# Optimization experiments

Hardware: AMD Instinct MI355X
Metric: run time of the kernel (lower is better)

Reference implementation:

```python
import jax, jax.numpy as jnp
import numpy as np

ALPHA = 0.9
EPS = 1e-5
SEQ, BATCH, D_MODEL, FF_DIM = 2048, 16, 512, 2048


def _layer_norm(x, g, b):
    m = jnp.mean(x, axis=-1, keepdims=True)
    v = jnp.mean((x - m) ** 2, axis=-1, keepdims=True)
    return (x - m) * jax.lax.rsqrt(v + EPS) * g + b


def _decay_matrix(seq, dtype):
    # Closed form of the torch roll/flip/tril loop:
    #   W[i, j] = alpha^{i-j+1}            for j <= i
    #   W[i, i] += 1 - sum_{k=1}^{i+1} alpha^k   (diag correction)
    i = jnp.arange(seq)
    diff = i[:, None] - i[None, :]                       # [S, S]
    causal = diff >= 0
    expo = jnp.where(causal, diff + 1, 0).astype(dtype)
    W = jnp.where(causal, jnp.asarray(ALPHA, dtype) ** expo, 0.0)
    W = W + jnp.diag(1.0 - W.sum(axis=1))
    return W


def setup_inputs() -> dict:
    key = jax.random.key(0)
    ks = jax.random.split(key, 8)
    s = lambda fan: 1.0 / np.sqrt(fan)
    return {
        "x": jax.random.normal(ks[0], (SEQ, BATCH, D_MODEL), jnp.float32),
        "w_lin": jax.random.normal(ks[1], (D_MODEL, D_MODEL), jnp.float32) * s(D_MODEL),
        "b_lin": jax.random.normal(ks[2], (D_MODEL,), jnp.float32) * 0.01,
        "w1": jax.random.normal(ks[3], (FF_DIM, D_MODEL), jnp.float32) * s(D_MODEL),
        "b1": jax.random.normal(ks[4], (FF_DIM,), jnp.float32) * 0.01,
        "w2": jax.random.normal(ks[5], (D_MODEL, FF_DIM), jnp.float32) * s(FF_DIM),
        "b2": jax.random.normal(ks[6], (D_MODEL,), jnp.float32) * 0.01,
        "g1": jnp.ones((D_MODEL,), jnp.float32),
        "beta1": jnp.zeros((D_MODEL,), jnp.float32),
        "g2": jnp.ones((D_MODEL,), jnp.float32),
        "beta2": jnp.zeros((D_MODEL,), jnp.float32),
    }


def reference(x, w_lin, b_lin, w1, b1, w2, b2, g1, beta1, g2, beta2):
    seq = x.shape[0]
    W = _decay_matrix(seq, x.dtype)                      # [S, S]

    # attention sublayer (dropout = identity in eval)
    y = _layer_norm(x, g1, beta1)
    z = jnp.einsum("sbd,ed->sbe", y, w_lin) + b_lin       # projection
    attn = jnp.einsum("ih,hbd->ibd", W, z)                # causal exp-decay mixing
    x = x + attn

    # feed-forward sublayer
    y = _layer_norm(x, g2, beta2)
    h = jax.nn.relu(jnp.einsum("sbd,fd->sbf", y, w1) + b1)
    ff = jnp.einsum("sbf,df->sbd", h, w2) + b2
    return x + ff
```

## Files before the change

kernel.cpp:

```cpp
#include <hip/hip_runtime.h>

#define SEQ 2048
#define BATCH 16
#define DMODEL 512
#define FFDIM 2048
#define NTOK (SEQ * BATCH)
#define ALPHA 0.9f

typedef unsigned short u16;
typedef unsigned int u32;
typedef __attribute__((ext_vector_type(8))) short short8;
typedef __attribute__((ext_vector_type(4))) float f32x4;

__device__ __forceinline__ float bf2f(u16 u) {
    unsigned int v = ((unsigned int)u) << 16;
    return __builtin_bit_cast(float, v);
}
__device__ __forceinline__ u16 f2bf(float f) {
    unsigned int v = __builtin_bit_cast(unsigned int, f);
    v += 0x7fffu + ((v >> 16) & 1u);
    return (u16)(v >> 16);
}

__global__ __launch_bounds__(256) void cvt_kernel(const float* __restrict__ in,
                                                  u16* __restrict__ out, int n) {
    const int i = (blockIdx.x * 256 + threadIdx.x) * 4;
    if (i >= n) return;
    float4 v = *(const float4*)(in + i);
    ushort4 o;
    o.x = f2bf(v.x); o.y = f2bf(v.y); o.z = f2bf(v.z); o.w = f2bf(v.w);
    *(ushort4*)(out + i) = o;
}

__global__ __launch_bounds__(256) void ln_kernel(const float* __restrict__ xin,
                                                 const float* __restrict__ g,
                                                 const float* __restrict__ b,
                                                 u16* __restrict__ y) {
    const int lane = threadIdx.x & 63;
    const int wave = threadIdx.x >> 6;
    const long tok = (long)blockIdx.x * 4 + wave;
    const long off = tok * DMODEL + lane * 8;

    float f[8];
    {
        const float4* xp = (const float4*)(xin + off);
        float4 a = xp[0], c = xp[1];
        f[0] = a.x; f[1] = a.y; f[2] = a.z; f[3] = a.w;
        f[4] = c.x; f[5] = c.y; f[6] = c.z; f[7] = c.w;
    }
    float s = 0.f, s2 = 0.f;
#pragma unroll
    for (int i = 0; i < 8; i++) { s += f[i]; s2 += f[i] * f[i]; }
#pragma unroll
    for (int o = 32; o > 0; o >>= 1) {
        s += __shfl_xor(s, o, 64);
        s2 += __shfl_xor(s2, o, 64);
    }
    const float mean = s * (1.f / DMODEL);
    const float var = s2 * (1.f / DMODEL) - mean * mean;
    const float inv = rsqrtf(var + 1e-5f);

    const float4* gp = (const float4*)(g + lane * 8);
    const float4* bp = (const float4*)(b + lane * 8);
    float4 g0 = gp[0], g1 = gp[1], b0 = bp[0], b1 = bp[1];
    float gg[8] = {g0.x, g0.y, g0.z, g0.w, g1.x, g1.y, g1.z, g1.w};
    float bb[8] = {b0.x, b0.y, b0.z, b0.w, b1.x, b1.y, b1.z, b1.w};
    short8 ov;
#pragma unroll
    for (int i = 0; i < 8; i++)
        ov[i] = (short)f2bf((f[i] - mean) * inv * gg[i] + bb[i]);
    *(short8*)(y + off) = ov;
}

#define SCAN_L 64
#define SCAN_H 128
#define NCOLU (BATCH * DMODEL / 2)
__global__ __launch_bounds__(256) void scan_kernel(const u16* __restrict__ z,
                                                   const float* __restrict__ x,
                                                   float* __restrict__ x1) {
    const int colu = blockIdx.x * 256 + threadIdx.x;
    const int s0 = blockIdx.y * SCAN_L;

    const u32* zp = (const u32*)z;
    const float2* xp = (const float2*)x;
    float2* x1p = (float2*)x1;

    float r0 = 0.f, r1 = 0.f;

    {
        int sb = s0 - SCAN_H;
        if (sb < 0) sb = 0;
        const int nw = s0 - sb;
        if (nw > 0) {
            u32 zq[4];
#pragma unroll
            for (int j = 0; j < 4; j++) zq[j] = zp[(long)(sb + j) * NCOLU + colu];
            for (int i = 0; i < nw; i += 4) {
#pragma unroll
                for (int j = 0; j < 4; j++) {
                    const u32 zz = zq[j];
                    if (i + j + 4 < nw)
                        zq[j] = zp[(long)(sb + i + j + 4) * NCOLU + colu];
                    r0 = ALPHA * (bf2f((u16)(zz & 0xffffu)) + r0);
                    r1 = ALPHA * (bf2f((u16)(zz >> 16)) + r1);
                }
            }
        }
    }

    float ap = powf(ALPHA, (float)(s0 + 2));

    u32 zq[4];
    float2 xq[4];
#pragma unroll
    for (int j = 0; j < 4; j++) {
        zq[j] = zp[(long)(s0 + j) * NCOLU + colu];
        xq[j] = xp[(long)(s0 + j) * NCOLU + colu];
    }
#pragma unroll 4
    for (int i = 0; i < SCAN_L; i++) {
        const int sl = i & 3;
        const u32 zz = zq[sl];
        const float2 xx = xq[sl];
        if (i + 4 < SCAN_L) {
            zq[sl] = zp[(long)(s0 + i + 4) * NCOLU + colu];
            xq[sl] = xp[(long)(s0 + i + 4) * NCOLU + colu];
        }
        const float z0 = bf2f((u16)(zz & 0xffffu));
        const float z1 = bf2f((u16)(zz >> 16));
        r0 = ALPHA * (z0 + r0);
        r1 = ALPHA * (z1 + r1);
        const float c = 1.f - (ALPHA - ap) * 10.f;
        ap *= ALPHA;
        x1p[(long)(s0 + i) * NCOLU + colu] = (float2){xx.x + r0 + c * z0, xx.y + r1 + c * z1};
    }
}

#define BM 128
#define BN 128
#define BKK 64

typedef __attribute__((address_space(1))) unsigned int as1_u32;
typedef __attribute__((address_space(3))) unsigned int as3_u32;

__device__ __forceinline__ void gld_lds16(const void* g, const void* l) {
    __builtin_amdgcn_global_load_lds((as1_u32*)(unsigned long long)g,
                                     (as3_u32*)(unsigned int)(unsigned long long)l,
                                     16, 0, 0);
}

template <int EPI, bool OUT_F32>
__global__ __launch_bounds__(256, 2) void gemm128(const u16* __restrict__ A,
                                                  const u16* __restrict__ Bt,
                                                  const float* __restrict__ bias,
                                                  const float* __restrict__ resid,
                                                  void* __restrict__ C,
                                                  int M, int N, int K) {
    __shared__ alignas(16) u16 sA[2][BM * BKK];
    __shared__ alignas(16) u16 sB[2][BN * BKK];

    const int tid = threadIdx.x;
    const int lane = tid & 63;
    const int wave = tid >> 6;
    const int wr = wave >> 1;
    const int wc = wave & 1;
    const int l15 = lane & 15, q16 = lane >> 4;

    const int gy = gridDim.y;
    const int nwg = gridDim.x * gy;
    const int d = blockIdx.y * gridDim.x + blockIdx.x;
    const int wgid = (d & 7) * (nwg >> 3) + (d >> 3);
    const int m0 = (wgid / gy) * BM;
    const int n0 = (wgid % gy) * BN;

    const u16* gA[4];
    const u16* gB[4];
    int ldsoff[4];
#pragma unroll
    for (int i = 0; i < 4; i++) {
        const int ch = tid + i * 256;
        const int r = ch >> 3;
        const int oo = (ch & 7) ^ (r & 7);
        gA[i] = A + (long)(m0 + r) * K + oo * 8;
        gB[i] = Bt + (long)(n0 + r) * K + oo * 8;
        ldsoff[i] = ch * 8;
    }

    const int x7 = l15 & 7;
    int octk[2];
    octk[0] = ((0 + q16) ^ x7) * 8;
    octk[1] = ((4 + q16) ^ x7) * 8;
    const int rowA0 = wr * 64 + l15;
    const int rowB0 = wc * 64 + l15;

    f32x4 acc[4][4];
#pragma unroll
    for (int i = 0; i < 4; i++)
#pragma unroll
        for (int j = 0; j < 4; j++) acc[i][j] = (f32x4){0.f, 0.f, 0.f, 0.f};

    const int NT = K / BKK;

#pragma unroll
    for (int i = 0; i < 4; i++) gld_lds16(gA[i], &sA[0][ldsoff[i]]);
#pragma unroll
    for (int i = 0; i < 4; i++) gld_lds16(gB[i], &sB[0][ldsoff[i]]);

#pragma unroll 1
    for (int t = 0; t < NT; ++t) {
        const int pb = t & 1;
        if (t + 1 < NT) {
            const int pn = (t + 1) & 1;
            const int ko = (t + 1) * BKK;
#pragma unroll
            for (int i = 0; i < 4; i++) gld_lds16(gA[i] + ko, &sA[pn][ldsoff[i]]);
#pragma unroll
            for (int i = 0; i < 4; i++) gld_lds16(gB[i] + ko, &sB[pn][ldsoff[i]]);
            asm volatile("s_waitcnt vmcnt(8)" ::: "memory");
        } else {
            asm volatile("s_waitcnt vmcnt(0)" ::: "memory");
        }
        __builtin_amdgcn_s_barrier();

        const u16* pa = &sA[pb][rowA0 * BKK];
        const u16* pbb = &sB[pb][rowB0 * BKK];

#pragma unroll
        for (int kk = 0; kk < 2; kk++) {
            short8 a[4], b[4];
#pragma unroll
            for (int i = 0; i < 4; i++)
                a[i] = *(const short8*)(pa + i * 16 * BKK + octk[kk]);
#pragma unroll
            for (int j = 0; j < 4; j++)
                b[j] = *(const short8*)(pbb + j * 16 * BKK + octk[kk]);
#pragma unroll
            for (int i = 0; i < 4; i++)
#pragma unroll
                for (int j = 0; j < 4; j++)
                    acc[i][j] = __builtin_amdgcn_mfma_f32_16x16x32_bf16(a[i], b[j],
                                                                        acc[i][j], 0, 0, 0);
        }
        __builtin_amdgcn_s_barrier();
    }

#pragma unroll
    for (int i = 0; i < 4; i++) {
        const int row0 = m0 + wr * 64 + i * 16 + q16 * 4;
#pragma unroll
        for (int j = 0; j < 4; j++) {
            const int col = n0 + wc * 64 + j * 16 + l15;
            const float bv = bias[col];
#pragma unroll
            for (int r = 0; r < 4; r++) {
                const long idx = (long)(row0 + r) * N + col;
                float v = acc[i][j][r] + bv;
                if (EPI == 1) v = fmaxf(v, 0.f);
                if (EPI == 2) v += resid[idx];
                if (OUT_F32)
                    ((float*)C)[idx] = v;
                else
                    ((u16*)C)[idx] = f2bf(v);
            }
        }
    }
}

extern "C" void kernel_launch(void* const* d_in, const int* in_sizes, int n_in,
                              void* d_out, int out_size, void* d_ws, size_t ws_size,
                              hipStream_t stream) {
    const float* x = (const float*)d_in[0];
    const float* w_lin = (const float*)d_in[1];
    const float* b_lin = (const float*)d_in[2];
    const float* w1 = (const float*)d_in[3];
    const float* b1 = (const float*)d_in[4];
    const float* w2 = (const float*)d_in[5];
    const float* b2 = (const float*)d_in[6];
    const float* g1 = (const float*)d_in[7];
    const float* be1 = (const float*)d_in[8];
    const float* g2 = (const float*)d_in[9];
    const float* be2 = (const float*)d_in[10];
    float* out = (float*)d_out;

    char* ws = (char*)d_ws;
    const size_t MB = 1024 * 1024;
    u16* y = (u16*)(ws);
    float* x1 = (float*)(ws + 32 * MB);
    u16* h = (u16*)(ws + 96 * MB);
    u16* z = h;
    u16* wb_lin = (u16*)(ws + 224 * MB);
    u16* wb1 = (u16*)(ws + 225 * MB);
    u16* wb2 = (u16*)(ws + 228 * MB);

    cvt_kernel<<<(DMODEL * DMODEL) / 1024, 256, 0, stream>>>(w_lin, wb_lin, DMODEL * DMODEL);
    cvt_kernel<<<(FFDIM * DMODEL) / 1024, 256, 0, stream>>>(w1, wb1, FFDIM * DMODEL);
    cvt_kernel<<<(DMODEL * FFDIM) / 1024, 256, 0, stream>>>(w2, wb2, DMODEL * FFDIM);

    ln_kernel<<<NTOK / 4, 256, 0, stream>>>(x, g1, be1, y);
    gemm128<0, false><<<dim3(NTOK / BM, DMODEL / BN), 256, 0, stream>>>(y, wb_lin, b_lin, nullptr,
                                                                       z, NTOK, DMODEL, DMODEL);
    scan_kernel<<<dim3(NCOLU / 256, SEQ / SCAN_L), 256, 0, stream>>>(z, x, x1);
    ln_kernel<<<NTOK / 4, 256, 0, stream>>>(x1, g2, be2, y);
    gemm128<1, false><<<dim3(NTOK / BM, FFDIM / BN), 256, 0, stream>>>(y, wb1, b1, nullptr, h,
                                                                      NTOK, FFDIM, DMODEL);
    gemm128<2, true><<<dim3(NTOK / BM, DMODEL / BN), 256, 0, stream>>>(h, wb2, b2, x1, out,
                                                                      NTOK, DMODEL, FFDIM);
}
```

Measured before the change: 437.4 us.

## Triple-buffer GEMM K-tiles at half depth and raise occupancy to three blocks

The bf16 MFMA GEMM's K-tile shrinks from 64 to 32 and the LDS ring grows from two to three stages, so global-to-LDS loads run two tiles ahead. The vmcnt waits and the XOR swizzle are adjusted to the narrower rows. Launch bounds ask for three blocks per CU, since per-block LDS drops from 64KB to 48KB. The aim is better latency hiding through deeper prefetch and more resident waves. The cost is twice as many barriers and loop iterations per unit of K, with less MFMA work between syncs.

```diff
diff --git a/kernel.cpp b/kernel.cpp
--- a/kernel.cpp
+++ b/kernel.cpp
@@ -138,7 +138,7 @@
 
 #define BM 128
 #define BN 128
-#define BKK 64
+#define BKK 32
 
 typedef __attribute__((address_space(1))) unsigned int as1_u32;
 typedef __attribute__((address_space(3))) unsigned int as3_u32;
@@ -150,14 +150,14 @@
 }
 
 template <int EPI, bool OUT_F32>
-__global__ __launch_bounds__(256, 2) void gemm128(const u16* __restrict__ A,
+__global__ __launch_bounds__(256, 3) void gemm128(const u16* __restrict__ A,
                                                   const u16* __restrict__ Bt,
                                                   const float* __restrict__ bias,
                                                   const float* __restrict__ resid,
                                                   void* __restrict__ C,
                                                   int M, int N, int K) {
-    __shared__ alignas(16) u16 sA[2][BM * BKK];
-    __shared__ alignas(16) u16 sB[2][BN * BKK];
+    __shared__ alignas(16) u16 sA[3][BM * BKK];
+    __shared__ alignas(16) u16 sB[3][BN * BKK];
 
     const int tid = threadIdx.x;
     const int lane = tid & 63;
@@ -173,23 +173,20 @@
     const int m0 = (wgid / gy) * BM;
     const int n0 = (wgid % gy) * BN;
 
-    const u16* gA[4];
-    const u16* gB[4];
-    int ldsoff[4];
-#pragma unroll
-    for (int i = 0; i < 4; i++) {
+    const u16* gA[2];
+    const u16* gB[2];
+    int ldsoff[2];
+#pragma unroll
+    for (int i = 0; i < 2; i++) {
         const int ch = tid + i * 256;
-        const int r = ch >> 3;
-        const int oo = (ch & 7) ^ (r & 7);
+        const int r = ch >> 2;
+        const int oo = (ch & 3) ^ ((r >> 1) & 3);
         gA[i] = A + (long)(m0 + r) * K + oo * 8;
         gB[i] = Bt + (long)(n0 + r) * K + oo * 8;
         ldsoff[i] = ch * 8;
     }
 
-    const int x7 = l15 & 7;
-    int octk[2];
-    octk[0] = ((0 + q16) ^ x7) * 8;
-    octk[1] = ((4 + q16) ^ x7) * 8;
+    const int octk = (q16 ^ ((l15 >> 1) & 3)) * 8;
     const int rowA0 = wr * 64 + l15;
     const int rowB0 = wc * 64 + l15;
 
@@ -202,46 +199,48 @@
     const int NT = K / BKK;
 
 #pragma unroll
-    for (int i = 0; i < 4; i++) gld_lds16(gA[i], &sA[0][ldsoff[i]]);
-#pragma unroll
-    for (int i = 0; i < 4; i++) gld_lds16(gB[i], &sB[0][ldsoff[i]]);
-
+    for (int i = 0; i < 2; i++) gld_lds16(gA[i], &sA[0][ldsoff[i]]);
+#pragma unroll
+    for (int i = 0; i < 2; i++) gld_lds16(gB[i], &sB[0][ldsoff[i]]);
+#pragma unroll
+    for (int i = 0; i < 2; i++) gld_lds16(gA[i] + BKK, &sA[1][ldsoff[i]]);
+#pragma unroll
+    for (int i = 0; i < 2; i++) gld_lds16(gB[i] + BKK, &sB[1][ldsoff[i]]);
+
+    int pb = 0;
 #pragma unroll 1
     for (int t = 0; t < NT; ++t) {
-        const int pb = t & 1;
-        if (t + 1 < NT) {
-            const int pn = (t + 1) & 1;
-            const int ko = (t + 1) * BKK;
-#pragma unroll
-            for (int i = 0; i < 4; i++) gld_lds16(gA[i] + ko, &sA[pn][ldsoff[i]]);
-#pragma unroll
-            for (int i = 0; i < 4; i++) gld_lds16(gB[i] + ko, &sB[pn][ldsoff[i]]);
+        if (t + 2 < NT) {
+            int ps = pb + 2; if (ps >= 3) ps -= 3;
+            const int ko = (t + 2) * BKK;
+#pragma unroll
+            for (int i = 0; i < 2; i++) gld_lds16(gA[i] + ko, &sA[ps][ldsoff[i]]);
+#pragma unroll
+            for (int i = 0; i < 2; i++) gld_lds16(gB[i] + ko, &sB[ps][ldsoff[i]]);
             asm volatile("s_waitcnt vmcnt(8)" ::: "memory");
+        } else if (t + 1 < NT) {
+            asm volatile("s_waitcnt vmcnt(4)" ::: "memory");
         } else {
             asm volatile("s_waitcnt vmcnt(0)" ::: "memory");
         }
         __builtin_amdgcn_s_barrier();
 
-        const u16* pa = &sA[pb][rowA0 * BKK];
-        const u16* pbb = &sB[pb][rowB0 * BKK];
-
-#pragma unroll
-        for (int kk = 0; kk < 2; kk++) {
-            short8 a[4], b[4];
-#pragma unroll
-            for (int i = 0; i < 4; i++)
-                a[i] = *(const short8*)(pa + i * 16 * BKK + octk[kk]);
+        const u16* pa = &sA[pb][rowA0 * BKK + octk];
+        const u16* pbb = &sB[pb][rowB0 * BKK + octk];
+
+        short8 a[4], b[4];
+#pragma unroll
+        for (int i = 0; i < 4; i++) a[i] = *(const short8*)(pa + i * 16 * BKK);
+#pragma unroll
+        for (int j = 0; j < 4; j++) b[j] = *(const short8*)(pbb + j * 16 * BKK);
+#pragma unroll
+        for (int i = 0; i < 4; i++)
 #pragma unroll
             for (int j = 0; j < 4; j++)
-                b[j] = *(const short8*)(pbb + j * 16 * BKK + octk[kk]);
-#pragma unroll
-            for (int i = 0; i < 4; i++)
-#pragma unroll
-                for (int j = 0; j < 4; j++)
-                    acc[i][j] = __builtin_amdgcn_mfma_f32_16x16x32_bf16(a[i], b[j],
-                                                                        acc[i][j], 0, 0, 0);
-        }
+                acc[i][j] = __builtin_amdgcn_mfma_f32_16x16x32_bf16(a[i], b[j],
+                                                                    acc[i][j], 0, 0, 0);
         __builtin_amdgcn_s_barrier();
+        pb = (pb == 2) ? 0 : pb + 1;
     }
 
 #pragma unroll
```

After: 444.1 us. About the same (+1.5%).

## Stage only A in LDS and load B fragments directly from global memory

Applied to the files above, without the earlier changes.

Reworks the GEMM into a 128x256 tile with 8 waves per block. Only the A tile is staged into LDS through swizzled direct-to-LDS loads; each wave reads its B (weight) fragments straight from global memory into registers. The aim is to halve LDS traffic and staging, relying on the cache to serve the reused weight matrix. In exchange, global-load latency now sits inside the MFMA loop with no prefetch for B.

```diff
diff --git a/kernel.cpp b/kernel.cpp
--- a/kernel.cpp
+++ b/kernel.cpp
@@ -137,7 +137,7 @@
 }
 
 #define BM 128
-#define BN 128
+#define BN 256
 #define BKK 64
 
 typedef __attribute__((address_space(1))) unsigned int as1_u32;
@@ -150,20 +150,19 @@
 }
 
 template <int EPI, bool OUT_F32>
-__global__ __launch_bounds__(256, 2) void gemm128(const u16* __restrict__ A,
-                                                  const u16* __restrict__ Bt,
-                                                  const float* __restrict__ bias,
-                                                  const float* __restrict__ resid,
-                                                  void* __restrict__ C,
-                                                  int M, int N, int K) {
-    __shared__ alignas(16) u16 sA[2][BM * BKK];
-    __shared__ alignas(16) u16 sB[2][BN * BKK];
+__global__ __launch_bounds__(512, 4) void gemm_bl2(const u16* __restrict__ A,
+                                                   const u16* __restrict__ Bt,
+                                                   const float* __restrict__ bias,
+                                                   const float* __restrict__ resid,
+                                                   void* __restrict__ C,
+                                                   int M, int N, int K) {
+    __shared__ alignas(16) u16 sA[2][2][128 * 32];
 
     const int tid = threadIdx.x;
     const int lane = tid & 63;
     const int wave = tid >> 6;
-    const int wr = wave >> 1;
-    const int wc = wave & 1;
+    const int wr = wave >> 2;
+    const int wc = wave & 3;
     const int l15 = lane & 15, q16 = lane >> 4;
 
     const int gy = gridDim.y;
@@ -173,25 +172,13 @@
     const int m0 = (wgid / gy) * BM;
     const int n0 = (wgid % gy) * BN;
 
-    const u16* gA[4];
-    const u16* gB[4];
-    int ldsoff[4];
-#pragma unroll
-    for (int i = 0; i < 4; i++) {
-        const int ch = tid + i * 256;
-        const int r = ch >> 3;
-        const int oo = (ch & 7) ^ (r & 7);
-        gA[i] = A + (long)(m0 + r) * K + oo * 8;
-        gB[i] = Bt + (long)(n0 + r) * K + oo * 8;
-        ldsoff[i] = ch * 8;
-    }
-
-    const int x7 = l15 & 7;
-    int octk[2];
-    octk[0] = ((0 + q16) ^ x7) * 8;
-    octk[1] = ((4 + q16) ^ x7) * 8;
-    const int rowA0 = wr * 64 + l15;
-    const int rowB0 = wc * 64 + l15;
+    const int c = (tid & 3) ^ ((tid >> 3) & 3);
+    const u16* gA0 = A + (long)(m0 + (tid >> 2)) * K + c * 8;
+    u16* dst0 = &sA[0][0][tid * 8];
+    const int dbufStride = 2 * 128 * 32;
+
+    const int xoct = (q16 ^ ((l15 >> 1) & 3)) * 8;
+    const u16* gB0 = Bt + (long)(n0 + wc * 64 + l15) * K + q16 * 8;
 
     f32x4 acc[4][4];
 #pragma unroll
@@ -201,60 +188,58 @@
 
     const int NT = K / BKK;
 
-#pragma unroll
-    for (int i = 0; i < 4; i++) gld_lds16(gA[i], &sA[0][ldsoff[i]]);
-#pragma unroll
-    for (int i = 0; i < 4; i++) gld_lds16(gB[i], &sB[0][ldsoff[i]]);
+#define STG_A(bs, koff)                                                     \
+    {                                                                       \
+        gld_lds16(gA0 + (koff), dst0 + (bs)*dbufStride);                    \
+        gld_lds16(gA0 + (koff) + 32, dst0 + (bs)*dbufStride + 128 * 32);    \
+    }
+
+    STG_A(0, 0);
 
 #pragma unroll 1
     for (int t = 0; t < NT; ++t) {
-        const int pb = t & 1;
-        if (t + 1 < NT) {
-            const int pn = (t + 1) & 1;
-            const int ko = (t + 1) * BKK;
-#pragma unroll
-            for (int i = 0; i < 4; i++) gld_lds16(gA[i] + ko, &sA[pn][ldsoff[i]]);
-#pragma unroll
-            for (int i = 0; i < 4; i++) gld_lds16(gB[i] + ko, &sB[pn][ldsoff[i]]);
-            asm volatile("s_waitcnt vmcnt(8)" ::: "memory");
+        const int b = t & 1, bn = b ^ 1;
+        const bool nx = (t + 1 < NT);
+        if (nx) {
+            STG_A(bn, (t + 1) * BKK);
+            asm volatile("s_waitcnt vmcnt(2)" ::: "memory");
         } else {
             asm volatile("s_waitcnt vmcnt(0)" ::: "memory");
         }
         __builtin_amdgcn_s_barrier();
 
-        const u16* pa = &sA[pb][rowA0 * BKK];
-        const u16* pbb = &sB[pb][rowB0 * BKK];
-
 #pragma unroll
         for (int kk = 0; kk < 2; kk++) {
-            short8 a[4], b[4];
-#pragma unroll
-            for (int i = 0; i < 4; i++)
-                a[i] = *(const short8*)(pa + i * 16 * BKK + octk[kk]);
-#pragma unroll
-            for (int j = 0; j < 4; j++)
-                b[j] = *(const short8*)(pbb + j * 16 * BKK + octk[kk]);
-#pragma unroll
-            for (int i = 0; i < 4; i++)
-#pragma unroll
-                for (int j = 0; j < 4; j++)
-                    acc[i][j] = __builtin_amdgcn_mfma_f32_16x16x32_bf16(a[i], b[j],
-                                                                        acc[i][j], 0, 0, 0);
+            short8 bf[4];
+#pragma unroll
+            for (int nj = 0; nj < 4; nj++)
+                bf[nj] = *(const short8*)(gB0 + (long)nj * 16 * K + t * BKK + kk * 32);
+            short8 af[4];
+#pragma unroll
+            for (int mi = 0; mi < 4; mi++)
+                af[mi] = *(const short8*)(&sA[b][kk][(wr * 64 + mi * 16 + l15) * 32 + xoct]);
+#pragma unroll
+            for (int mi = 0; mi < 4; mi++)
+#pragma unroll
+                for (int nj = 0; nj < 4; nj++)
+                    acc[mi][nj] = __builtin_amdgcn_mfma_f32_16x16x32_bf16(af[mi], bf[nj],
+                                                                          acc[mi][nj], 0, 0, 0);
         }
         __builtin_amdgcn_s_barrier();
     }
-
-#pragma unroll
-    for (int i = 0; i < 4; i++) {
-        const int row0 = m0 + wr * 64 + i * 16 + q16 * 4;
-#pragma unroll
-        for (int j = 0; j < 4; j++) {
-            const int col = n0 + wc * 64 + j * 16 + l15;
+#undef STG_A
+
+#pragma unroll
+    for (int mi = 0; mi < 4; mi++) {
+        const int row0 = m0 + wr * 64 + mi * 16 + q16 * 4;
+#pragma unroll
+        for (int nj = 0; nj < 4; nj++) {
+            const int col = n0 + wc * 64 + nj * 16 + l15;
             const float bv = bias[col];
 #pragma unroll
             for (int r = 0; r < 4; r++) {
                 const long idx = (long)(row0 + r) * N + col;
-                float v = acc[i][j][r] + bv;
+                float v = acc[mi][nj][r] + bv;
                 if (EPI == 1) v = fmaxf(v, 0.f);
                 if (EPI == 2) v += resid[idx];
                 if (OUT_F32)
@@ -297,12 +282,13 @@
     cvt_kernel<<<(DMODEL * FFDIM) / 1024, 256, 0, stream>>>(w2, wb2, DMODEL * FFDIM);
 
     ln_kernel<<<NTOK / 4, 256, 0, stream>>>(x, g1, be1, y);
-    gemm128<0, false><<<dim3(NTOK / BM, DMODEL / BN), 256, 0, stream>>>(y, wb_lin, b_lin, nullptr,
-                                                                       z, NTOK, DMODEL, DMODEL);
+    gemm_bl2<0, false><<<dim3(NTOK / BM, DMODEL / BN), 512, 0, stream>>>(y, wb_lin, b_lin,
+                                                                        nullptr, z,
+                                                                        NTOK, DMODEL, DMODEL);
     scan_kernel<<<dim3(NCOLU / 256, SEQ / SCAN_L), 256, 0, stream>>>(z, x, x1);
     ln_kernel<<<NTOK / 4, 256, 0, stream>>>(x1, g2, be2, y);
-    gemm128<1, false><<<dim3(NTOK / BM, FFDIM / BN), 256, 0, stream>>>(y, wb1, b1, nullptr, h,
-                                                                      NTOK, FFDIM, DMODEL);
-    gemm128<2, true><<<dim3(NTOK / BM, DMODEL / BN), 256, 0, stream>>>(h, wb2, b2, x1, out,
-                                                                      NTOK, DMODEL, FFDIM);
-}
+    gemm_bl2<1, false><<<dim3(NTOK / BM, FFDIM / BN), 512, 0, stream>>>(y, wb1, b1, nullptr, h,
+                                                                       NTOK, FFDIM, DMODEL);
+    gemm_bl2<2, true><<<dim3(NTOK / BM, DMODEL / BN), 512, 0, stream>>>(h, wb2, b2, x1, out,
+                                                                       NTOK, DMODEL, FFDIM);
+}
```

Measured after the change: 567.2 us. 29.7% more time.
